# Performance work log

Measured on AMD Instinct MI355X. Metric: run time of the kernel, lower is better.

Reference implementation:

```python
import jax, jax.numpy as jnp
import numpy as np

C_IN = 128
DIM = 2 * C_IN          # ELAN final channels = 2*in_channels = 256
WS = 8                  # window size
HEADS = 8
HEAD_DIM = DIM // HEADS
B, H, W = 4, 128, 128
LN_EPS = 1e-5


def setup_inputs() -> dict:
    key = jax.random.key(0)
    ks = jax.random.split(key, 20)
    mid = C_IN // 2  # middle_channels == block_channels == 64

    def p(k, shape, scale=0.05):
        return jax.random.normal(k, shape, jnp.float32) * scale

    return dict(
        x=jax.random.normal(ks[0], (B, C_IN, H, W), jnp.float32),
        # ELAN stem 1x1 convs: [main, short], each folded BN (scale, bias)
        w_stem=p(ks[1], (2, mid, C_IN, 1, 1)),
        s_stem=1.0 + p(ks[2], (2, mid)),
        b_stem=p(ks[3], (2, mid)),
        # 2 blocks x 2 convs of 3x3, mid->mid
        w_blk=p(ks[4], (4, mid, mid, 3, 3)),
        s_blk=1.0 + p(ks[5], (4, mid)),
        b_blk=p(ks[6], (4, mid)),
        # SwinV2 block params
        norm1_g=jnp.ones((DIM,), jnp.float32),
        norm1_b=jnp.zeros((DIM,), jnp.float32),
        qkv_w=p(ks[7], (3 * DIM, DIM)),
        qkv_b=p(ks[8], (3 * DIM,)).at[DIM:2 * DIM].set(0.0),  # V2 zeroes k bias
        proj_w=p(ks[9], (DIM, DIM)),
        proj_b=p(ks[10], (DIM,)),
        logit_scale=jnp.full((HEADS, 1, 1), float(np.log(10.0)), jnp.float32),
        cpb_w1=p(ks[11], (512, 2)),
        cpb_b1=p(ks[12], (512,)),
        cpb_w2=p(ks[13], (HEADS, 512)),
        norm2_g=jnp.ones((DIM,), jnp.float32),
        norm2_b=jnp.zeros((DIM,), jnp.float32),
        mlp_w1=p(ks[14], (DIM, DIM)),  # mlp_ratio=1.0
        mlp_b1=p(ks[15], (DIM,)),
        mlp_w2=p(ks[16], (DIM, DIM)),
        mlp_b2=p(ks[17], (DIM,)),
    )


def convbn(x, w, s, b, pad):
    # Conv(no bias) + eval-mode BN folded into per-channel scale/bias + SiLU
    y = jax.lax.conv_general_dilated(
        x, w, (1, 1), [(pad, pad), (pad, pad)],
        dimension_numbers=("NCHW", "OIHW", "NCHW"))
    y = y * s[None, :, None, None] + b[None, :, None, None]
    return jax.nn.silu(y)


def layernorm(x, g, b):
    m = jnp.mean(x, -1, keepdims=True)
    v = jnp.var(x, -1, keepdims=True)
    return (x - m) * jax.lax.rsqrt(v + LN_EPS) * g + b


def _rel_bias_consts():
    ws = WS
    ch = np.arange(-(ws - 1), ws, dtype=np.float32)
    table = np.stack(np.meshgrid(ch, ch, indexing="ij"), axis=-1)  # [2ws-1,2ws-1,2]
    table = table / (ws - 1) * 8.0
    table = np.sign(table) * np.log2(np.abs(table) + 1.0) / 3.0
    coords = np.stack(np.meshgrid(np.arange(ws), np.arange(ws), indexing="ij")).reshape(2, -1)
    rel = (coords[:, :, None] - coords[:, None, :]).transpose(1, 2, 0)  # [N,N,2]
    rel[..., 0] += ws - 1
    rel[..., 1] += ws - 1
    rel[..., 0] *= 2 * ws - 1
    idx = rel.sum(-1).reshape(-1)
    return jnp.asarray(table.reshape(-1, 2)), jnp.asarray(idx)


_TABLE, _IDX = _rel_bias_consts()


def elan_swin(x, w_stem, s_stem, b_stem, w_blk, s_blk, b_blk, norm1_g, norm1_b,
              qkv_w, qkv_b, proj_w, proj_b, logit_scale, cpb_w1, cpb_b1, cpb_w2,
              norm2_g, norm2_b, mlp_w1, mlp_b1, mlp_w2, mlp_b2):
    # ---- ELANBlock ----
    x_short = convbn(x, w_stem[1], s_stem[1], b_stem[1], 0)
    x_main = convbn(x, w_stem[0], s_stem[0], b_stem[0], 0)
    xb = x_main
    outs = []
    for i in range(2):
        xb = convbn(xb, w_blk[2 * i], s_blk[2 * i], b_blk[2 * i], 1)
        xb = convbn(xb, w_blk[2 * i + 1], s_blk[2 * i + 1], b_blk[2 * i + 1], 1)
        outs.append(xb)
    e = jnp.concatenate([outs[1], outs[0], x_main, x_short], axis=1)  # [B,DIM,H,W]
    e = e.transpose(0, 2, 3, 1)  # NHWC

    # ---- ShiftedWindowAttentionV2 (shift=0, H,W divisible by WS) ----
    Bn, Hh, Ww, Cc = e.shape
    nH, nW = Hh // WS, Ww // WS
    N = WS * WS
    xw = e.reshape(Bn, nH, WS, nW, WS, Cc).transpose(0, 1, 3, 2, 4, 5).reshape(-1, N, Cc)
    qkv = xw @ qkv_w.T + qkv_b
    qkv = qkv.reshape(-1, N, 3, HEADS, HEAD_DIM).transpose(2, 0, 3, 1, 4)
    q, k, v = qkv[0], qkv[1], qkv[2]  # [Bw, heads, N, d]
    qn = q / jnp.maximum(jnp.linalg.norm(q, axis=-1, keepdims=True), 1e-12)
    kn = k / jnp.maximum(jnp.linalg.norm(k, axis=-1, keepdims=True), 1e-12)
    attn = jnp.einsum("whnd,whmd->whnm", qn, kn)
    scale = jnp.exp(jnp.minimum(logit_scale, jnp.log(100.0)))  # [heads,1,1]
    attn = attn * scale[None]
    # continuous position bias MLP
    bias = jax.nn.relu(_TABLE @ cpb_w1.T + cpb_b1) @ cpb_w2.T  # [(2ws-1)^2, heads]
    bias = bias[_IDX].reshape(N, N, HEADS).transpose(2, 0, 1)
    bias = 16.0 * jax.nn.sigmoid(bias)
    attn = jax.nn.softmax(attn + bias[None], axis=-1)
    out = jnp.einsum("whnm,whmd->whnd", attn, v).transpose(0, 2, 1, 3).reshape(-1, N, Cc)
    out = out @ proj_w.T + proj_b
    out = out.reshape(Bn, nH, nW, WS, WS, Cc).transpose(0, 1, 3, 2, 4, 5).reshape(Bn, Hh, Ww, Cc)

    # ---- SwinTransformerBlockV2 (post-norm residuals) ----
    s = e + layernorm(out, norm1_g, norm1_b)
    h = s @ mlp_w1.T + mlp_b1
    h = jax.nn.gelu(h, approximate=False)
    h = h @ mlp_w2.T + mlp_b2
    s = s + layernorm(h, norm2_g, norm2_b)
    return s.transpose(0, 3, 1, 2)  # NCHW


def reference(x, w_stem, s_stem, b_stem, w_blk, s_blk, b_blk, norm1_g, norm1_b,
              qkv_w, qkv_b, proj_w, proj_b, logit_scale, cpb_w1, cpb_b1, cpb_w2,
              norm2_g, norm2_b, mlp_w1, mlp_b1, mlp_w2, mlp_b2):
    return elan_swin(x, w_stem, s_stem, b_stem, w_blk, s_blk, b_blk, norm1_g, norm1_b,
                     qkv_w, qkv_b, proj_w, proj_b, logit_scale, cpb_w1, cpb_b1, cpb_w2,
                     norm2_g, norm2_b, mlp_w1, mlp_b1, mlp_w2, mlp_b2)
```

## Files before the change

kernel.cpp:

```cpp
#include <hip/hip_runtime.h>
#include <hip/hip_bf16.h>
#include <math.h>


#define HW 16384
typedef unsigned int u32;
typedef unsigned short u16;
typedef __attribute__((ext_vector_type(8))) short short8;
typedef __attribute__((ext_vector_type(4))) float floatx4;

#define MEMBAR() asm volatile("" ::: "memory")

__device__ __forceinline__ float silu_f(float y) { return y / (1.f + expf(-y)); }
__device__ __forceinline__ float bflo(u32 u) { return __uint_as_float(u << 16); }
__device__ __forceinline__ float bfhi(u32 u) { return __uint_as_float(u & 0xffff0000u); }
__device__ __forceinline__ float bf2f(u16 v) { return __uint_as_float((u32)v << 16); }
__device__ __forceinline__ u16 f2bf(float x) {
  u32 u = __float_as_uint(x);
  u += 0x7fffu + ((u >> 16) & 1u);
  return (u16)(u >> 16);
}
__device__ __forceinline__ u32 pack2(float a, float b) {
  return (u32)f2bf(a) | ((u32)f2bf(b) << 16);
}

#define GLDS16(gp, lp)                                           \
  __builtin_amdgcn_global_load_lds(                              \
      (const __attribute__((address_space(1))) void*)(gp),       \
      (__attribute__((address_space(3))) void*)(lp), 16, 0, 0)

__global__ __launch_bounds__(256) void repack_kernel(
    const float* __restrict__ w_blk, const float* __restrict__ s_blk,
    const float* __restrict__ w_stem, const float* __restrict__ s_stem,
    u16* __restrict__ wtc, u16* __restrict__ wts) {
  int idx = blockIdx.x * 256 + threadIdx.x;
  if (idx < 147456) {
    int c = idx & 63;
    int rest = idx >> 6;
    int oc = rest & 63;
    int ct = rest >> 6;
    int conv = ct / 9, t = ct % 9;
    float w = w_blk[((size_t)(conv * 64 + oc) * 64 + c) * 9 + t];
    wtc[idx] = f2bf(w * s_blk[conv * 64 + oc]);
  } else if (idx < 147456 + 16384) {
    int j = idx - 147456;
    int c = j & 127, oc = j >> 7;
    float w = w_stem[(size_t)oc * 128 + c];
    wts[j] = f2bf(w * s_stem[oc]);
  }
}

__global__ __launch_bounds__(256) void castw_kernel(
    const float* __restrict__ in, u16* __restrict__ outp, int n) {
  int i = blockIdx.x * 256 + threadIdx.x;
  if (i < n) outp[i] = f2bf(in[i]);
}

__global__ __launch_bounds__(512) void cpb_mlp_kernel(
    const float* __restrict__ w1, const float* __restrict__ b1,
    const float* __restrict__ w2, float* __restrict__ pre) {
  __shared__ float hb[512];
  int t = blockIdx.x, j = threadIdx.x;
  int i = t / 15, jj = t % 15;
  float c0 = (float)(i - 7) * (8.f / 7.f);
  float c1 = (float)(jj - 7) * (8.f / 7.f);
  float s0 = (c0 > 0.f) ? 1.f : ((c0 < 0.f) ? -1.f : 0.f);
  float s1 = (c1 > 0.f) ? 1.f : ((c1 < 0.f) ? -1.f : 0.f);
  float t0 = s0 * log2f(fabsf(c0) + 1.f) * (1.f / 3.f);
  float t1 = s1 * log2f(fabsf(c1) + 1.f) * (1.f / 3.f);
  float h = t0 * w1[j * 2] + t1 * w1[j * 2 + 1] + b1[j];
  hb[j] = fmaxf(h, 0.f);
  __syncthreads();
  if (j < 8) {
    float s = 0.f;
    for (int k = 0; k < 512; ++k) s += hb[k] * w2[j * 512 + k];
    pre[t * 8 + j] = s;
  }
}

__global__ __launch_bounds__(256) void cpb_expand_kernel(
    const float* __restrict__ pre, float* __restrict__ bias_t) {
  int idx = blockIdx.x * 256 + threadIdx.x;
  int m = idx >> 6, n = idx & 63;
  int di = (n >> 3) - (m >> 3) + 7;
  int dj = (n & 7) - (m & 7) + 7;
  int ti = di * 15 + dj;
#pragma unroll
  for (int h = 0; h < 8; ++h) {
    float v = pre[ti * 8 + h];
    bias_t[h * 4096 + idx] = 16.f / (1.f + expf(-v));
  }
}

__global__ __launch_bounds__(256) void transpose_in_kernel(
    const float* __restrict__ x, u16* __restrict__ xt) {
  __shared__ float tl[64][65];
  int bid = blockIdx.x;
  int b = bid >> 9;
  int r = bid & 511;
  int cs = r >> 8, hws = r & 255;
  int c0 = cs << 6, hw0 = hws << 6;
  int tid = threadIdx.x;
  for (int e = tid; e < 4096; e += 256) {
    int c = e >> 6, p = e & 63;
    tl[c][p] = x[(size_t)(b * 128 + c0 + c) * HW + hw0 + p];
  }
  __syncthreads();
  for (int e = tid; e < 4096; e += 256) {
    int p = e >> 6, c = e & 63;
    xt[(size_t)(b * HW + hw0 + p) * 128 + c0 + c] = f2bf(tl[c][p]);
  }
}

__global__ __launch_bounds__(256, 4) void gemm_bf16_kernel(
    const u16* __restrict__ A, const u16* __restrict__ W,
    const float* __restrict__ bias, u16* __restrict__ C, int K, int ldc,
    int act) {
  __shared__ u16 As[128 * 64];
  __shared__ u16 Ws[64 * 64];
  int tid = threadIdx.x;
  int wv = tid >> 6, lane = tid & 63;
  int m0 = blockIdx.y * 128, n0 = blockIdx.x * 64;
  floatx4 zz = {0.f, 0.f, 0.f, 0.f};
  floatx4 acc[2][4];
#pragma unroll
  for (int i = 0; i < 2; ++i)
#pragma unroll
    for (int j = 0; j < 4; ++j) acc[i][j] = zz;
  int lr = lane >> 3, ls = lane & 7;
  for (int k0 = 0; k0 < K; k0 += 64) {
#pragma unroll
    for (int i = 0; i < 4; ++i) {
      int ci = wv * 4 + i;
      int r = ci * 8 + lr;
      int cc = ls ^ (r & 7);
      GLDS16(A + (size_t)(m0 + r) * K + k0 + cc * 8, As + ci * 512);
    }
#pragma unroll
    for (int i = 0; i < 2; ++i) {
      int ci = wv * 2 + i;
      int r = ci * 8 + lr;
      int cc = ls ^ (r & 7);
      GLDS16(W + (size_t)(n0 + r) * K + k0 + cc * 8, Ws + ci * 512);
    }
    __syncthreads();
#pragma unroll
    for (int kk = 0; kk < 2; ++kk) {
      int g = kk * 4 + (lane >> 4);
      short8 a0, a1, b0, b1, b2, b3;
      {
        int row = wv * 32 + (lane & 15);
        a0 = *(const short8*)&As[row * 64 + (g ^ (row & 7)) * 8];
        int row2 = row + 16;
        a1 = *(const short8*)&As[row2 * 64 + (g ^ (row2 & 7)) * 8];
      }
      {
        int col = lane & 15;
        b0 = *(const short8*)&Ws[col * 64 + (g ^ (col & 7)) * 8];
        int c1 = col + 16;
        b1 = *(const short8*)&Ws[c1 * 64 + (g ^ (c1 & 7)) * 8];
        int c2 = col + 32;
        b2 = *(const short8*)&Ws[c2 * 64 + (g ^ (c2 & 7)) * 8];
        int c3 = col + 48;
        b3 = *(const short8*)&Ws[c3 * 64 + (g ^ (c3 & 7)) * 8];
      }
      acc[0][0] = __builtin_amdgcn_mfma_f32_16x16x32_bf16(a0, b0, acc[0][0], 0, 0, 0);
      acc[0][1] = __builtin_amdgcn_mfma_f32_16x16x32_bf16(a0, b1, acc[0][1], 0, 0, 0);
      acc[0][2] = __builtin_amdgcn_mfma_f32_16x16x32_bf16(a0, b2, acc[0][2], 0, 0, 0);
      acc[0][3] = __builtin_amdgcn_mfma_f32_16x16x32_bf16(a0, b3, acc[0][3], 0, 0, 0);
      acc[1][0] = __builtin_amdgcn_mfma_f32_16x16x32_bf16(a1, b0, acc[1][0], 0, 0, 0);
      acc[1][1] = __builtin_amdgcn_mfma_f32_16x16x32_bf16(a1, b1, acc[1][1], 0, 0, 0);
      acc[1][2] = __builtin_amdgcn_mfma_f32_16x16x32_bf16(a1, b2, acc[1][2], 0, 0, 0);
      acc[1][3] = __builtin_amdgcn_mfma_f32_16x16x32_bf16(a1, b3, acc[1][3], 0, 0, 0);
    }
    __syncthreads();
  }
  int rbase = wv * 32 + ((lane >> 4) << 2);
  int cb = lane & 15;
#pragma unroll
  for (int mi = 0; mi < 2; ++mi) {
#pragma unroll
    for (int nj = 0; nj < 4; ++nj) {
      int col = n0 + nj * 16 + cb;
      float bv = bias[col];
#pragma unroll
      for (int r = 0; r < 4; ++r) {
        int row = m0 + rbase + mi * 16 + r;
        float v = acc[mi][nj][r] + bv;
        if (act == 1) v = 0.5f * v * (1.f + erff(v * 0.70710678118654752f));
        else if (act == 2) v = silu_f(v);
        C[(size_t)row * ldc + col] = f2bf(v);
      }
    }
  }
}

__global__ __launch_bounds__(256) void conv3x3_mfma_kernel(
    const u16* __restrict__ in, int istr, u16* __restrict__ outp, int ostr,
    const u16* __restrict__ wt, const float* __restrict__ bias) {
  __shared__ u16 tile[6400];
  int tid = threadIdx.x;
  int wv = tid >> 6, lane = tid & 63;
  int bx = blockIdx.x, by = blockIdx.y, b = blockIdx.z;
  int h0 = by * 8, w0 = bx * 8;
#pragma unroll
  for (int rr = 0; rr < 4; ++rr) {
    int slot = rr * 256 + tid;
    int p = slot >> 3, ch = slot & 7;
    if (p < 100) {
      int hr = p / 10, hc = p % 10;
      int gh = h0 + hr - 1, gw = w0 + hc - 1;
      bool ok = (gh >= 0) && (gh < 128) && (gw >= 0) && (gw < 128);
      uint4 v = {0u, 0u, 0u, 0u};
      if (ok) {
        size_t pix = (size_t)((b * 128 + gh) * 128 + gw);
        v = *(const uint4*)(in + pix * istr + ch * 8);
      }
      *(uint4*)(tile + p * 64 + ((ch ^ (p & 7)) << 3)) = v;
    }
  }
  __syncthreads();
  int pl = lane & 15;
  int g = lane >> 4;
  int prow = 2 * wv + (pl >> 3), pcol = pl & 7;
  floatx4 zz = {0.f, 0.f, 0.f, 0.f};
  floatx4 acc[4] = {zz, zz, zz, zz};
#pragma unroll
  for (int t = 0; t < 9; ++t) {
    int dy = t / 3, dx = t % 3;
    int hp = (prow + dy) * 10 + (pcol + dx);
    short8 bf0 = *(const short8*)&tile[hp * 64 + (((0 * 4 + g) ^ (hp & 7)) << 3)];
    short8 bf1 = *(const short8*)&tile[hp * 64 + (((1 * 4 + g) ^ (hp & 7)) << 3)];
    const u16* wtap = wt + t * 4096;
#pragma unroll
    for (int nf = 0; nf < 4; ++nf) {
      short8 a0 = *(const short8*)&wtap[(nf * 16 + pl) * 64 + g * 8];
      short8 a1 = *(const short8*)&wtap[(nf * 16 + pl) * 64 + 32 + g * 8];
      acc[nf] = __builtin_amdgcn_mfma_f32_16x16x32_bf16(a0, bf0, acc[nf], 0, 0, 0);
      acc[nf] = __builtin_amdgcn_mfma_f32_16x16x32_bf16(a1, bf1, acc[nf], 0, 0, 0);
    }
  }
  size_t pix = (size_t)((b * 128 + h0 + prow) * 128 + w0 + pcol);
#pragma unroll
  for (int nf = 0; nf < 4; ++nf) {
    float o0 = silu_f(acc[nf][0] + bias[nf * 16 + g * 4 + 0]);
    float o1 = silu_f(acc[nf][1] + bias[nf * 16 + g * 4 + 1]);
    float o2 = silu_f(acc[nf][2] + bias[nf * 16 + g * 4 + 2]);
    float o3 = silu_f(acc[nf][3] + bias[nf * 16 + g * 4 + 3]);
    uint2 w2;
    w2.x = pack2(o0, o1);
    w2.y = pack2(o2, o3);
    *(uint2*)(outp + pix * ostr + nf * 16 + g * 4) = w2;
  }
}

__global__ __launch_bounds__(256) void attn_fused_kernel(
    const u16* __restrict__ ebf, const u16* __restrict__ qwb,
    const float* __restrict__ qkv_b, const float* __restrict__ logit_scale,
    const float* __restrict__ bias_t, u16* __restrict__ ao) {
  __shared__ __align__(16) char lds[73728];
  int tid = threadIdx.x;
  int w = tid >> 6, l = tid & 63;
  int wid = blockIdx.x >> 1;
  int h = __builtin_amdgcn_readfirstlane(((blockIdx.x & 1) << 2) + w);
  u16* Elds = (u16*)lds;
  char* Kn = lds + 32768 + w * 10240;
  char* Qn = Kn + 5120;
  char* Pt = Kn;
  char* Vt = lds + w * 4608;
  char* Ol = Vt;

  int b = wid >> 8, wh = (wid >> 4) & 15, ww = wid & 15;
  int pixbase = (b << 14) + wh * 1024 + ww * 8;
  {
    int lr = l >> 3, ls = l & 7;
#pragma unroll
    for (int j = 0; j < 8; ++j) {
      int pix = pixbase + j * 128 + lr;
      GLDS16(ebf + (size_t)pix * 256 + w * 64 + ((ls ^ lr) << 3),
             Elds + (w * 8 + j) * 512);
    }
  }
  __syncthreads();

  int lc = l & 15, lg = l >> 4;
  float scale = __expf(fminf(logit_scale[h], 4.6051701860f));

  floatx4 zz = {0.f, 0.f, 0.f, 0.f};
  floatx4 aq[4][2], ak[4][2], av[4][2];
#pragma unroll
  for (int mf = 0; mf < 4; ++mf) {
    aq[mf][0] = zz; aq[mf][1] = zz;
    ak[mf][0] = zz; ak[mf][1] = zz;
    av[mf][0] = zz; av[mf][1] = zz;
  }
#pragma unroll
  for (int ks = 0; ks < 8; ++ks) {
    int ch = ks >> 1, g = ((ks & 1) << 2) + lg;
    short8 af[4];
#pragma unroll
    for (int mf = 0; mf < 4; ++mf) {
      int tk = mf * 16 + lc;
      af[mf] = *(const short8*)&Elds[(ch * 64 + tk) * 64 + ((g ^ (tk & 7)) << 3)];
    }
#pragma unroll
    for (int nf = 0; nf < 2; ++nf) {
      const u16* wb = qwb + (size_t)(h * 32 + nf * 16 + lc) * 256 + ks * 32 + lg * 8;
      short8 bq = *(const short8*)(wb);
      short8 bk = *(const short8*)(wb + 65536);
      short8 bv = *(const short8*)(wb + 131072);
#pragma unroll
      for (int mf = 0; mf < 4; ++mf) {
        aq[mf][nf] = __builtin_amdgcn_mfma_f32_16x16x32_bf16(af[mf], bq, aq[mf][nf], 0, 0, 0);
        ak[mf][nf] = __builtin_amdgcn_mfma_f32_16x16x32_bf16(af[mf], bk, ak[mf][nf], 0, 0, 0);
        av[mf][nf] = __builtin_amdgcn_mfma_f32_16x16x32_bf16(af[mf], bv, av[mf][nf], 0, 0, 0);
      }
    }
  }
  __syncthreads();

  {
    float vb0 = qkv_b[512 + h * 32 + lc], vb1 = qkv_b[512 + h * 32 + 16 + lc];
#pragma unroll
    for (int mf = 0; mf < 4; ++mf)
#pragma unroll
      for (int r = 0; r < 4; ++r) {
        int tk = mf * 16 + (lg << 2) + r;
        *(u16*)(Vt + lc * 144 + tk * 2) = f2bf(av[mf][0][r] + vb0);
        *(u16*)(Vt + (16 + lc) * 144 + tk * 2) = f2bf(av[mf][1][r] + vb1);
      }
  }
  MEMBAR();

  short8 kf[4], qf[4];
#pragma unroll
  for (int mf = 0; mf < 4; ++mf)
#pragma unroll
    for (int r = 0; r < 4; ++r) {
      float v0 = ak[mf][0][r], v1 = ak[mf][1][r];
      float ss = v0 * v0 + v1 * v1;
      ss += __shfl_xor(ss, 1);
      ss += __shfl_xor(ss, 2);
      ss += __shfl_xor(ss, 4);
      ss += __shfl_xor(ss, 8);
      float rk = 1.f / fmaxf(sqrtf(ss), 1e-12f);
      int tk = mf * 16 + (lg << 2) + r;
      *(u16*)(Kn + tk * 80 + lc * 2) = f2bf(v0 * rk);
      *(u16*)(Kn + tk * 80 + (16 + lc) * 2) = f2bf(v1 * rk);
    }
  MEMBAR();
#pragma unroll
  for (int i = 0; i < 4; ++i)
    kf[i] = *(const short8*)(Kn + (i * 16 + lc) * 80 + (lg << 4));
  MEMBAR();

  {
    float qb0 = qkv_b[h * 32 + lc], qb1 = qkv_b[h * 32 + 16 + lc];
#pragma unroll
    for (int mf = 0; mf < 4; ++mf)
#pragma unroll
      for (int r = 0; r < 4; ++r) {
        float v0 = aq[mf][0][r] + qb0, v1 = aq[mf][1][r] + qb1;
        float ss = v0 * v0 + v1 * v1;
        ss += __shfl_xor(ss, 1);
        ss += __shfl_xor(ss, 2);
        ss += __shfl_xor(ss, 4);
        ss += __shfl_xor(ss, 8);
        float rq = scale / fmaxf(sqrtf(ss), 1e-12f);
        int tk = mf * 16 + (lg << 2) + r;
        *(u16*)(Qn + tk * 80 + lc * 2) = f2bf(v0 * rq);
        *(u16*)(Qn + tk * 80 + (16 + lc) * 2) = f2bf(v1 * rq);
      }
    MEMBAR();
#pragma unroll
    for (int i = 0; i < 4; ++i)
      qf[i] = *(const short8*)(Qn + (i * 16 + lc) * 80 + (lg << 4));
    MEMBAR();
  }

  floatx4 S[4][4];
#pragma unroll
  for (int mi = 0; mi < 4; ++mi)
#pragma unroll
    for (int ni = 0; ni < 4; ++ni)
      S[mi][ni] = __builtin_amdgcn_mfma_f32_16x16x32_bf16(kf[mi], qf[ni], zz, 0, 0, 0);

  const float* bh = bias_t + h * 4096;
  float den[4] = {0.f, 0.f, 0.f, 0.f};
#pragma unroll
  for (int mi = 0; mi < 4; ++mi) {
    int mb = mi * 16 + (lg << 2);
#pragma unroll
    for (int ni = 0; ni < 4; ++ni) {
      int nn = ni * 16 + lc;
#pragma unroll
      for (int r = 0; r < 4; ++r) {
        float e = __expf(S[mi][ni][r] + bh[(mb + r) * 64 + nn]);
        S[mi][ni][r] = e;
        den[ni] += e;
      }
    }
  }
#pragma unroll
  for (int ni = 0; ni < 4; ++ni) {
    den[ni] += __shfl_xor(den[ni], 16);
    den[ni] += __shfl_xor(den[ni], 32);
    den[ni] = 1.f / den[ni];
  }
#pragma unroll
  for (int ni = 0; ni < 4; ++ni)
#pragma unroll
    for (int mi = 0; mi < 4; ++mi) {
      uint2 v;
      v.x = pack2(S[mi][ni][0] * den[ni], S[mi][ni][1] * den[ni]);
      v.y = pack2(S[mi][ni][2] * den[ni], S[mi][ni][3] * den[ni]);
      *(uint2*)(Pt + (ni * 16 + lc) * 144 + mi * 32 + (lg << 3)) = v;
    }
  MEMBAR();
  short8 vf[2][2];
#pragma unroll
  for (int ks = 0; ks < 2; ++ks)
#pragma unroll
    for (int db = 0; db < 2; ++db)
      vf[ks][db] = *(const short8*)(Vt + (db * 16 + lc) * 144 + ks * 64 + (lg << 4));
  floatx4 O[4][2];
#pragma unroll
  for (int nb = 0; nb < 4; ++nb) {
    O[nb][0] = zz;
    O[nb][1] = zz;
  }
#pragma unroll
  for (int nb = 0; nb < 4; ++nb) {
    short8 pf0 = *(const short8*)(Pt + (nb * 16 + lc) * 144 + (lg << 4));
    short8 pf1 = *(const short8*)(Pt + (nb * 16 + lc) * 144 + 64 + (lg << 4));
    O[nb][0] = __builtin_amdgcn_mfma_f32_16x16x32_bf16(pf0, vf[0][0], O[nb][0], 0, 0, 0);
    O[nb][0] = __builtin_amdgcn_mfma_f32_16x16x32_bf16(pf1, vf[1][0], O[nb][0], 0, 0, 0);
    O[nb][1] = __builtin_amdgcn_mfma_f32_16x16x32_bf16(pf0, vf[0][1], O[nb][1], 0, 0, 0);
    O[nb][1] = __builtin_amdgcn_mfma_f32_16x16x32_bf16(pf1, vf[1][1], O[nb][1], 0, 0, 0);
  }
  MEMBAR();
#pragma unroll
  for (int nb = 0; nb < 4; ++nb)
#pragma unroll
    for (int r = 0; r < 4; ++r) {
      int n = nb * 16 + (lg << 2) + r;
      *(u16*)(Ol + n * 72 + lc * 2) = f2bf(O[nb][0][r]);
      *(u16*)(Ol + n * 72 + (16 + lc) * 2) = f2bf(O[nb][1][r]);
    }
  MEMBAR();
  u32 ov[16];
#pragma unroll
  for (int j = 0; j < 16; ++j) ov[j] = *(const u32*)(Ol + l * 72 + j * 4);
  uint4* op = (uint4*)(ao + (size_t)(wid * 64 + l) * 256 + h * 32);
#pragma unroll
  for (int q4 = 0; q4 < 4; ++q4) {
    uint4 v;
    v.x = ov[q4 * 4 + 0];
    v.y = ov[q4 * 4 + 1];
    v.z = ov[q4 * 4 + 2];
    v.w = ov[q4 * 4 + 3];
    op[q4] = v;
  }
}

__global__ __launch_bounds__(256) void ln1v_kernel(
    const u16* __restrict__ pin, const u16* __restrict__ ebf,
    u16* __restrict__ sbf, const float* __restrict__ g,
    const float* __restrict__ bb) {
  int tid = threadIdx.x;
  int bid = blockIdx.x;
  int b = bid >> 8, hw0 = (bid & 255) << 6;
  int i = tid >> 2, qq = tid & 3;
  int hw = hw0 + i;
  int him = hw >> 7, wim = hw & 127;
  int wid = b * 256 + (him >> 3) * 16 + (wim >> 3);
  int t = wid * 64 + (him & 7) * 8 + (wim & 7);
  size_t pbase = (size_t)t * 256 + qq * 64;
  size_t ebase = ((size_t)(b * HW + hw)) * 256 + qq * 64;
  float v[64];
  float s1 = 0.f, s2 = 0.f;
#pragma unroll
  for (int j = 0; j < 8; ++j) {
    uint4 u = *(const uint4*)(pin + pbase + j * 8);
    u32 ua[4] = {u.x, u.y, u.z, u.w};
#pragma unroll
    for (int k = 0; k < 4; ++k) {
      float a = bflo(ua[k]), c = bfhi(ua[k]);
      v[j * 8 + 2 * k] = a;
      v[j * 8 + 2 * k + 1] = c;
      s1 += a + c;
      s2 += a * a + c * c;
    }
  }
  s1 += __shfl_xor(s1, 1);
  s1 += __shfl_xor(s1, 2);
  s2 += __shfl_xor(s2, 1);
  s2 += __shfl_xor(s2, 2);
  float mean = s1 * (1.f / 256.f);
  float var = s2 * (1.f / 256.f) - mean * mean;
  float rs = rsqrtf(var + 1e-5f);
#pragma unroll
  for (int j = 0; j < 8; ++j) {
    uint4 u = *(const uint4*)(ebf + ebase + j * 8);
    u32 ua[4] = {u.x, u.y, u.z, u.w};
    uint4 o;
    u32 ow[4];
#pragma unroll
    for (int k = 0; k < 4; ++k) {
      int c = qq * 64 + j * 8 + 2 * k;
      float o0 = bflo(ua[k]) + (v[j * 8 + 2 * k] - mean) * rs * g[c] + bb[c];
      float o1 = bfhi(ua[k]) + (v[j * 8 + 2 * k + 1] - mean) * rs * g[c + 1] + bb[c + 1];
      ow[k] = pack2(o0, o1);
    }
    o.x = ow[0]; o.y = ow[1]; o.z = ow[2]; o.w = ow[3];
    *(uint4*)(sbf + ebase + j * 8) = o;
  }
}

__global__ __launch_bounds__(256) void ln2t_kernel(
    const u16* __restrict__ h2, const u16* __restrict__ sbf,
    const float* __restrict__ g, const float* __restrict__ bb,
    float* __restrict__ outp) {
  __shared__ float tile[64][257];
  int tid = threadIdx.x;
  int bid = blockIdx.x;
  int b = bid >> 8, hw0 = (bid & 255) << 6;
  int i = tid >> 2, qq = tid & 3;
  size_t base = ((size_t)(b * HW + hw0 + i)) * 256 + qq * 64;
  float v[64];
  float s1 = 0.f, s2 = 0.f;
#pragma unroll
  for (int j = 0; j < 8; ++j) {
    uint4 u = *(const uint4*)(h2 + base + j * 8);
    u32 ua[4] = {u.x, u.y, u.z, u.w};
#pragma unroll
    for (int k = 0; k < 4; ++k) {
      float a = bflo(ua[k]), c = bfhi(ua[k]);
      v[j * 8 + 2 * k] = a;
      v[j * 8 + 2 * k + 1] = c;
      s1 += a + c;
      s2 += a * a + c * c;
    }
  }
  s1 += __shfl_xor(s1, 1);
  s1 += __shfl_xor(s1, 2);
  s2 += __shfl_xor(s2, 1);
  s2 += __shfl_xor(s2, 2);
  float mean = s1 * (1.f / 256.f);
  float var = s2 * (1.f / 256.f) - mean * mean;
  float rs = rsqrtf(var + 1e-5f);
#pragma unroll
  for (int j = 0; j < 8; ++j) {
    uint4 u = *(const uint4*)(sbf + base + j * 8);
    u32 ua[4] = {u.x, u.y, u.z, u.w};
#pragma unroll
    for (int k = 0; k < 4; ++k) {
      int c = qq * 64 + j * 8 + 2 * k;
      tile[i][c] = bflo(ua[k]) + (v[j * 8 + 2 * k] - mean) * rs * g[c] + bb[c];
      tile[i][c + 1] = bfhi(ua[k]) + (v[j * 8 + 2 * k + 1] - mean) * rs * g[c + 1] + bb[c + 1];
    }
  }
  __syncthreads();
  int pl = tid & 63, cq = tid >> 6;
#pragma unroll 8
  for (int cc = 0; cc < 64; ++cc) {
    int c = cq * 64 + cc;
    outp[((size_t)(b * 256 + c)) * HW + hw0 + pl] = tile[pl][c];
  }
}

extern "C" void kernel_launch(void* const* d_in, const int* in_sizes, int n_in,
                              void* d_out, int out_size, void* d_ws, size_t ws_size,
                              hipStream_t stream) {
  const float* x        = (const float*)d_in[0];
  const float* w_stem   = (const float*)d_in[1];
  const float* s_stem   = (const float*)d_in[2];
  const float* b_stem   = (const float*)d_in[3];
  const float* w_blk    = (const float*)d_in[4];
  const float* s_blk    = (const float*)d_in[5];
  const float* b_blk    = (const float*)d_in[6];
  const float* norm1_g  = (const float*)d_in[7];
  const float* norm1_b  = (const float*)d_in[8];
  const float* qkv_w    = (const float*)d_in[9];
  const float* qkv_b    = (const float*)d_in[10];
  const float* proj_w   = (const float*)d_in[11];
  const float* proj_b   = (const float*)d_in[12];
  const float* logit_sc = (const float*)d_in[13];
  const float* cpb_w1   = (const float*)d_in[14];
  const float* cpb_b1   = (const float*)d_in[15];
  const float* cpb_w2   = (const float*)d_in[16];
  const float* norm2_g  = (const float*)d_in[17];
  const float* norm2_b  = (const float*)d_in[18];
  const float* mlp_w1   = (const float*)d_in[19];
  const float* mlp_b1   = (const float*)d_in[20];
  const float* mlp_w2   = (const float*)d_in[21];
  const float* mlp_b2   = (const float*)d_in[22];
  float* out = (float*)d_out;
  float* ws = (float*)d_ws;
  (void)in_sizes; (void)n_in; (void)out_size; (void)ws_size;

  float* R0 = ws;
  float* R1 = ws + 16777216;
  float* R2 = ws + 33554432;
  float* TAIL = ws + 50331648;
  u16* WTC  = (u16*)TAIL;
  u16* WTS  = (u16*)(TAIL + 73728);
  u16* QWB  = (u16*)(TAIL + 81920);
  u16* PWB  = (u16*)(TAIL + 180224);
  u16* M1WB = (u16*)(TAIL + 212992);
  u16* M2WB = (u16*)(TAIL + 245760);
  float* BPRE = TAIL + 278528;
  float* BFT  = TAIL + 280576;

  u16* XT  = (u16*)R2;
  u16* EBF = (u16*)(R2 + 8388608);
  u16* T1  = (u16*)R1;
  u16* T2  = (u16*)(R1 + 2097152);
  u16* AO  = (u16*)R0;
  u16* P   = (u16*)(R0 + 8388608);
  u16* SBF = (u16*)R0;
  u16* Hb  = (u16*)R2;
  u16* H2  = (u16*)(R0 + 8388608);

  repack_kernel<<<640, 256, 0, stream>>>(w_blk, s_blk, w_stem, s_stem, WTC, WTS);
  castw_kernel<<<768, 256, 0, stream>>>(qkv_w, QWB, 196608);
  castw_kernel<<<256, 256, 0, stream>>>(proj_w, PWB, 65536);
  castw_kernel<<<256, 256, 0, stream>>>(mlp_w1, M1WB, 65536);
  castw_kernel<<<256, 256, 0, stream>>>(mlp_w2, M2WB, 65536);
  cpb_mlp_kernel<<<225, 512, 0, stream>>>(cpb_w1, cpb_b1, cpb_w2, BPRE);
  cpb_expand_kernel<<<16, 256, 0, stream>>>(BPRE, BFT);

  transpose_in_kernel<<<2048, 256, 0, stream>>>(x, XT);
  dim3 gs(2, 512);
  gemm_bf16_kernel<<<gs, 256, 0, stream>>>(XT, WTS, b_stem, EBF + 128, 128, 256, 2);

  dim3 cgrid(16, 16, 4);
  conv3x3_mfma_kernel<<<cgrid, 256, 0, stream>>>(EBF + 128, 256, T1, 64, WTC, b_blk);
  conv3x3_mfma_kernel<<<cgrid, 256, 0, stream>>>(T1, 64, EBF + 64, 256, WTC + 9 * 4096, b_blk + 64);
  conv3x3_mfma_kernel<<<cgrid, 256, 0, stream>>>(EBF + 64, 256, T2, 64, WTC + 18 * 4096, b_blk + 128);
  conv3x3_mfma_kernel<<<cgrid, 256, 0, stream>>>(T2, 64, EBF, 256, WTC + 27 * 4096, b_blk + 192);

  attn_fused_kernel<<<2048, 256, 0, stream>>>(EBF, QWB, qkv_b, logit_sc, BFT, AO);

  dim3 g4(4, 512);
  gemm_bf16_kernel<<<g4, 256, 0, stream>>>(AO, PWB, proj_b, P, 256, 256, 0);
  ln1v_kernel<<<1024, 256, 0, stream>>>(P, EBF, SBF, norm1_g, norm1_b);
  gemm_bf16_kernel<<<g4, 256, 0, stream>>>(SBF, M1WB, mlp_b1, Hb, 256, 256, 1);
  gemm_bf16_kernel<<<g4, 256, 0, stream>>>(Hb, M2WB, mlp_b2, H2, 256, 256, 0);
  ln2t_kernel<<<1024, 256, 0, stream>>>(H2, SBF, norm2_g, norm2_b, out);
}
```

Measured before the change: 467.0 us.

## Split QKV projection into sequential passes and pass P/V via lane shuffles

The fused window-attention kernel now computes K, Q and V in three sequential MFMA passes that reuse one accumulator set instead of holding all three at once. P and V fragments are rearranged into MFMA operand layout with cross-lane shuffles rather than round-tripping through LDS. Together these shrink LDS from 72KB to 52KB and raise launch bounds to allow three blocks per CU. Separately, the GEMM grid axes are swapped so consecutive blocks walk along M, which changes L2 reuse of the weight tiles. The cost is three separate passes reading the E tile and weights from LDS and global, plus extra shuffle instructions.

```diff
diff --git a/kernel.cpp b/kernel.cpp
--- a/kernel.cpp
+++ b/kernel.cpp
@@ -22,6 +22,16 @@
 }
 __device__ __forceinline__ u32 pack2(float a, float b) {
   return (u32)f2bf(a) | ((u32)f2bf(b) << 16);
+}
+__device__ __forceinline__ short8 mk8(u32 a, u32 b, u32 c, u32 d) {
+  union { u32 u[4]; short8 s; } t;
+  t.u[0] = a; t.u[1] = b; t.u[2] = c; t.u[3] = d;
+  return t.s;
+}
+__device__ __forceinline__ u32 shfl_sel(u32 va, u32 vb, int s, bool sel) {
+  u32 x = (u32)__shfl((int)va, s);
+  u32 y = (u32)__shfl((int)vb, s);
+  return sel ? y : x;
 }
 
 #define GLDS16(gp, lp)                                           \
@@ -120,7 +130,7 @@
   __shared__ u16 Ws[64 * 64];
   int tid = threadIdx.x;
   int wv = tid >> 6, lane = tid & 63;
-  int m0 = blockIdx.y * 128, n0 = blockIdx.x * 64;
+  int m0 = blockIdx.x * 128, n0 = blockIdx.y * 64;
   floatx4 zz = {0.f, 0.f, 0.f, 0.f};
   floatx4 acc[2][4];
 #pragma unroll
@@ -254,21 +264,48 @@
   }
 }
 
-__global__ __launch_bounds__(256) void attn_fused_kernel(
+__device__ __forceinline__ void qkv_mm(const u16* Elds, const u16* qwb,
+                                       int moff, int h, int lc, int lg,
+                                       floatx4 acc[4][2]) {
+  floatx4 zz = {0.f, 0.f, 0.f, 0.f};
+#pragma unroll
+  for (int mf = 0; mf < 4; ++mf) {
+    acc[mf][0] = zz;
+    acc[mf][1] = zz;
+  }
+#pragma unroll
+  for (int ks = 0; ks < 8; ++ks) {
+    int ch = ks >> 1, g = ((ks & 1) << 2) + lg;
+    short8 af[4];
+#pragma unroll
+    for (int mf = 0; mf < 4; ++mf) {
+      int tk = mf * 16 + lc;
+      af[mf] = *(const short8*)&Elds[(ch * 64 + tk) * 64 + ((g ^ (tk & 7)) << 3)];
+    }
+#pragma unroll
+    for (int nf = 0; nf < 2; ++nf) {
+      short8 bf = *(const short8*)(qwb +
+          (size_t)(moff + h * 32 + nf * 16 + lc) * 256 + ks * 32 + lg * 8);
+#pragma unroll
+      for (int mf = 0; mf < 4; ++mf)
+        acc[mf][nf] =
+            __builtin_amdgcn_mfma_f32_16x16x32_bf16(af[mf], bf, acc[mf][nf], 0, 0, 0);
+    }
+  }
+}
+
+__global__ __launch_bounds__(256, 3) void attn_fused_kernel(
     const u16* __restrict__ ebf, const u16* __restrict__ qwb,
     const float* __restrict__ qkv_b, const float* __restrict__ logit_scale,
     const float* __restrict__ bias_t, u16* __restrict__ ao) {
-  __shared__ __align__(16) char lds[73728];
+  __shared__ __align__(16) char lds[53248];
   int tid = threadIdx.x;
   int w = tid >> 6, l = tid & 63;
   int wid = blockIdx.x >> 1;
   int h = __builtin_amdgcn_readfirstlane(((blockIdx.x & 1) << 2) + w);
   u16* Elds = (u16*)lds;
-  char* Kn = lds + 32768 + w * 10240;
-  char* Qn = Kn + 5120;
-  char* Pt = Kn;
-  char* Vt = lds + w * 4608;
-  char* Ol = Vt;
+  char* Sc = lds + 32768 + w * 5120;
+  char* Ol = lds + w * 8192;
 
   int b = wid >> 8, wh = (wid >> 4) & 15, ww = wid & 15;
   int pixbase = (b << 14) + wh * 1024 + ww * 8;
@@ -285,59 +322,15 @@
 
   int lc = l & 15, lg = l >> 4;
   float scale = __expf(fminf(logit_scale[h], 4.6051701860f));
-
-  floatx4 zz = {0.f, 0.f, 0.f, 0.f};
-  floatx4 aq[4][2], ak[4][2], av[4][2];
-#pragma unroll
-  for (int mf = 0; mf < 4; ++mf) {
-    aq[mf][0] = zz; aq[mf][1] = zz;
-    ak[mf][0] = zz; ak[mf][1] = zz;
-    av[mf][0] = zz; av[mf][1] = zz;
-  }
-#pragma unroll
-  for (int ks = 0; ks < 8; ++ks) {
-    int ch = ks >> 1, g = ((ks & 1) << 2) + lg;
-    short8 af[4];
-#pragma unroll
-    for (int mf = 0; mf < 4; ++mf) {
-      int tk = mf * 16 + lc;
-      af[mf] = *(const short8*)&Elds[(ch * 64 + tk) * 64 + ((g ^ (tk & 7)) << 3)];
-    }
-#pragma unroll
-    for (int nf = 0; nf < 2; ++nf) {
-      const u16* wb = qwb + (size_t)(h * 32 + nf * 16 + lc) * 256 + ks * 32 + lg * 8;
-      short8 bq = *(const short8*)(wb);
-      short8 bk = *(const short8*)(wb + 65536);
-      short8 bv = *(const short8*)(wb + 131072);
-#pragma unroll
-      for (int mf = 0; mf < 4; ++mf) {
-        aq[mf][nf] = __builtin_amdgcn_mfma_f32_16x16x32_bf16(af[mf], bq, aq[mf][nf], 0, 0, 0);
-        ak[mf][nf] = __builtin_amdgcn_mfma_f32_16x16x32_bf16(af[mf], bk, ak[mf][nf], 0, 0, 0);
-        av[mf][nf] = __builtin_amdgcn_mfma_f32_16x16x32_bf16(af[mf], bv, av[mf][nf], 0, 0, 0);
-      }
-    }
-  }
-  __syncthreads();
-
-  {
-    float vb0 = qkv_b[512 + h * 32 + lc], vb1 = qkv_b[512 + h * 32 + 16 + lc];
-#pragma unroll
-    for (int mf = 0; mf < 4; ++mf)
-#pragma unroll
-      for (int r = 0; r < 4; ++r) {
-        int tk = mf * 16 + (lg << 2) + r;
-        *(u16*)(Vt + lc * 144 + tk * 2) = f2bf(av[mf][0][r] + vb0);
-        *(u16*)(Vt + (16 + lc) * 144 + tk * 2) = f2bf(av[mf][1][r] + vb1);
-      }
-  }
-  MEMBAR();
-
+  floatx4 macc[4][2];
   short8 kf[4], qf[4];
+
+  qkv_mm(Elds, qwb, 256, h, lc, lg, macc);
 #pragma unroll
   for (int mf = 0; mf < 4; ++mf)
 #pragma unroll
     for (int r = 0; r < 4; ++r) {
-      float v0 = ak[mf][0][r], v1 = ak[mf][1][r];
+      float v0 = macc[mf][0][r], v1 = macc[mf][1][r];
       float ss = v0 * v0 + v1 * v1;
       ss += __shfl_xor(ss, 1);
       ss += __shfl_xor(ss, 2);
@@ -345,22 +338,23 @@
       ss += __shfl_xor(ss, 8);
       float rk = 1.f / fmaxf(sqrtf(ss), 1e-12f);
       int tk = mf * 16 + (lg << 2) + r;
-      *(u16*)(Kn + tk * 80 + lc * 2) = f2bf(v0 * rk);
-      *(u16*)(Kn + tk * 80 + (16 + lc) * 2) = f2bf(v1 * rk);
+      *(u16*)(Sc + tk * 80 + lc * 2) = f2bf(v0 * rk);
+      *(u16*)(Sc + tk * 80 + (16 + lc) * 2) = f2bf(v1 * rk);
     }
   MEMBAR();
 #pragma unroll
   for (int i = 0; i < 4; ++i)
-    kf[i] = *(const short8*)(Kn + (i * 16 + lc) * 80 + (lg << 4));
+    kf[i] = *(const short8*)(Sc + (i * 16 + lc) * 80 + (lg << 4));
   MEMBAR();
 
+  qkv_mm(Elds, qwb, 0, h, lc, lg, macc);
   {
     float qb0 = qkv_b[h * 32 + lc], qb1 = qkv_b[h * 32 + 16 + lc];
 #pragma unroll
     for (int mf = 0; mf < 4; ++mf)
 #pragma unroll
       for (int r = 0; r < 4; ++r) {
-        float v0 = aq[mf][0][r] + qb0, v1 = aq[mf][1][r] + qb1;
+        float v0 = macc[mf][0][r] + qb0, v1 = macc[mf][1][r] + qb1;
         float ss = v0 * v0 + v1 * v1;
         ss += __shfl_xor(ss, 1);
         ss += __shfl_xor(ss, 2);
@@ -368,16 +362,31 @@
         ss += __shfl_xor(ss, 8);
         float rq = scale / fmaxf(sqrtf(ss), 1e-12f);
         int tk = mf * 16 + (lg << 2) + r;
-        *(u16*)(Qn + tk * 80 + lc * 2) = f2bf(v0 * rq);
-        *(u16*)(Qn + tk * 80 + (16 + lc) * 2) = f2bf(v1 * rq);
+        *(u16*)(Sc + tk * 80 + lc * 2) = f2bf(v0 * rq);
+        *(u16*)(Sc + tk * 80 + (16 + lc) * 2) = f2bf(v1 * rq);
       }
     MEMBAR();
 #pragma unroll
     for (int i = 0; i < 4; ++i)
-      qf[i] = *(const short8*)(Qn + (i * 16 + lc) * 80 + (lg << 4));
+      qf[i] = *(const short8*)(Sc + (i * 16 + lc) * 80 + (lg << 4));
     MEMBAR();
   }
 
+  u32 v01[4][2], v23[4][2];
+  qkv_mm(Elds, qwb, 512, h, lc, lg, macc);
+  {
+    float vb0 = qkv_b[512 + h * 32 + lc], vb1 = qkv_b[512 + h * 32 + 16 + lc];
+#pragma unroll
+    for (int mf = 0; mf < 4; ++mf) {
+      v01[mf][0] = pack2(macc[mf][0][0] + vb0, macc[mf][0][1] + vb0);
+      v23[mf][0] = pack2(macc[mf][0][2] + vb0, macc[mf][0][3] + vb0);
+      v01[mf][1] = pack2(macc[mf][1][0] + vb1, macc[mf][1][1] + vb1);
+      v23[mf][1] = pack2(macc[mf][1][2] + vb1, macc[mf][1][3] + vb1);
+    }
+  }
+  __syncthreads();
+
+  floatx4 zz = {0.f, 0.f, 0.f, 0.f};
   floatx4 S[4][4];
 #pragma unroll
   for (int mi = 0; mi < 4; ++mi)
@@ -407,38 +416,50 @@
     den[ni] += __shfl_xor(den[ni], 32);
     den[ni] = 1.f / den[ni];
   }
-#pragma unroll
-  for (int ni = 0; ni < 4; ++ni)
-#pragma unroll
-    for (int mi = 0; mi < 4; ++mi) {
-      uint2 v;
-      v.x = pack2(S[mi][ni][0] * den[ni], S[mi][ni][1] * den[ni]);
-      v.y = pack2(S[mi][ni][2] * den[ni], S[mi][ni][3] * den[ni]);
-      *(uint2*)(Pt + (ni * 16 + lc) * 144 + mi * 32 + (lg << 3)) = v;
-    }
-  MEMBAR();
+  u32 p01[4][4], p23[4][4];
+#pragma unroll
+  for (int mi = 0; mi < 4; ++mi)
+#pragma unroll
+    for (int ni = 0; ni < 4; ++ni) {
+      p01[mi][ni] = pack2(S[mi][ni][0] * den[ni], S[mi][ni][1] * den[ni]);
+      p23[mi][ni] = pack2(S[mi][ni][2] * den[ni], S[mi][ni][3] * den[ni]);
+    }
+
+  int s1 = ((lg & 1) << 5) + lc;
+  int s2 = s1 + 16;
+  bool hi = lg >= 2;
   short8 vf[2][2];
 #pragma unroll
   for (int ks = 0; ks < 2; ++ks)
 #pragma unroll
-    for (int db = 0; db < 2; ++db)
-      vf[ks][db] = *(const short8*)(Vt + (db * 16 + lc) * 144 + ks * 64 + (lg << 4));
+    for (int db = 0; db < 2; ++db) {
+      u32 w0 = shfl_sel(v01[ks * 2][db], v01[ks * 2 + 1][db], s1, hi);
+      u32 w1 = shfl_sel(v23[ks * 2][db], v23[ks * 2 + 1][db], s1, hi);
+      u32 w2 = shfl_sel(v01[ks * 2][db], v01[ks * 2 + 1][db], s2, hi);
+      u32 w3 = shfl_sel(v23[ks * 2][db], v23[ks * 2 + 1][db], s2, hi);
+      vf[ks][db] = mk8(w0, w1, w2, w3);
+    }
   floatx4 O[4][2];
 #pragma unroll
   for (int nb = 0; nb < 4; ++nb) {
-    O[nb][0] = zz;
-    O[nb][1] = zz;
-  }
-#pragma unroll
-  for (int nb = 0; nb < 4; ++nb) {
-    short8 pf0 = *(const short8*)(Pt + (nb * 16 + lc) * 144 + (lg << 4));
-    short8 pf1 = *(const short8*)(Pt + (nb * 16 + lc) * 144 + 64 + (lg << 4));
-    O[nb][0] = __builtin_amdgcn_mfma_f32_16x16x32_bf16(pf0, vf[0][0], O[nb][0], 0, 0, 0);
-    O[nb][0] = __builtin_amdgcn_mfma_f32_16x16x32_bf16(pf1, vf[1][0], O[nb][0], 0, 0, 0);
-    O[nb][1] = __builtin_amdgcn_mfma_f32_16x16x32_bf16(pf0, vf[0][1], O[nb][1], 0, 0, 0);
-    O[nb][1] = __builtin_amdgcn_mfma_f32_16x16x32_bf16(pf1, vf[1][1], O[nb][1], 0, 0, 0);
-  }
-  MEMBAR();
+    u32 a0 = shfl_sel(p01[0][nb], p01[1][nb], s1, hi);
+    u32 a1 = shfl_sel(p23[0][nb], p23[1][nb], s1, hi);
+    u32 a2 = shfl_sel(p01[0][nb], p01[1][nb], s2, hi);
+    u32 a3 = shfl_sel(p23[0][nb], p23[1][nb], s2, hi);
+    short8 pf0 = mk8(a0, a1, a2, a3);
+    u32 b0 = shfl_sel(p01[2][nb], p01[3][nb], s1, hi);
+    u32 b1 = shfl_sel(p23[2][nb], p23[3][nb], s1, hi);
+    u32 b2 = shfl_sel(p01[2][nb], p01[3][nb], s2, hi);
+    u32 b3 = shfl_sel(p23[2][nb], p23[3][nb], s2, hi);
+    short8 pf1 = mk8(b0, b1, b2, b3);
+    floatx4 o0 = __builtin_amdgcn_mfma_f32_16x16x32_bf16(pf0, vf[0][0], zz, 0, 0, 0);
+    o0 = __builtin_amdgcn_mfma_f32_16x16x32_bf16(pf1, vf[1][0], o0, 0, 0, 0);
+    floatx4 o1 = __builtin_amdgcn_mfma_f32_16x16x32_bf16(pf0, vf[0][1], zz, 0, 0, 0);
+    o1 = __builtin_amdgcn_mfma_f32_16x16x32_bf16(pf1, vf[1][1], o1, 0, 0, 0);
+    O[nb][0] = o0;
+    O[nb][1] = o1;
+  }
+
 #pragma unroll
   for (int nb = 0; nb < 4; ++nb)
 #pragma unroll
@@ -631,7 +652,7 @@
   cpb_expand_kernel<<<16, 256, 0, stream>>>(BPRE, BFT);
 
   transpose_in_kernel<<<2048, 256, 0, stream>>>(x, XT);
-  dim3 gs(2, 512);
+  dim3 gs(512, 2);
   gemm_bf16_kernel<<<gs, 256, 0, stream>>>(XT, WTS, b_stem, EBF + 128, 128, 256, 2);
 
   dim3 cgrid(16, 16, 4);
@@ -642,7 +663,7 @@
 
   attn_fused_kernel<<<2048, 256, 0, stream>>>(EBF, QWB, qkv_b, logit_sc, BFT, AO);
 
-  dim3 g4(4, 512);
+  dim3 g4(512, 4);
   gemm_bf16_kernel<<<g4, 256, 0, stream>>>(AO, PWB, proj_b, P, 256, 256, 0);
   ln1v_kernel<<<1024, 256, 0, stream>>>(P, EBF, SBF, norm1_g, norm1_b);
   gemm_bf16_kernel<<<g4, 256, 0, stream>>>(SBF, M1WB, mlp_b1, Hb, 256, 256, 1);
```

After: 428.5 us. 8.2% less time.
